# Kernel tuning notes

Measured on AMD Instinct MI355X. Metric: run time of the kernel, lower is better.

## Reference

```python
import jax, jax.numpy as jnp
import numpy as np

B, S, D, H, DH, R = 8, 2048, 1024, 16, 64, 32
ALPHA, BETA, GAMMA = 0.2, 0.1, 0.1


def setup_inputs() -> dict:
    key = jax.random.key(0)
    ks = jax.random.split(key, 5)
    x = jax.random.normal(ks[0], (B, S, D), jnp.float32)
    q = jax.random.normal(ks[1], (B, S, H, DH), jnp.float32)
    k = jax.random.normal(ks[2], (B, S, H, DH), jnp.float32)
    v_value = jax.random.normal(ks[3], (B, S, D), jnp.float32)
    # reentry_proj weight (orthogonal init approximated by scaled gaussian)
    W = jax.random.normal(ks[4], (D, D), jnp.float32) * np.float32(np.sqrt(0.5 / D))
    return {"x": x, "q": q, "k": k, "v_value": v_value, "W": W}


def _normalize(t):
    return t / (jnp.linalg.norm(t, axis=-1, keepdims=True) + 1e-6)


def reference(x, q, k, v_value, W):
    Bz, Sl, Dm = x.shape
    qf = q.reshape(Bz, Sl, Dm).transpose(1, 0, 2)        # (S, B, D)
    kf = k.reshape(Bz, Sl, Dm).transpose(1, 0, 2)        # (S, B, D)
    vf = v_value.transpose(1, 0, 2)                      # (S, B, D)
    U0 = jnp.zeros((Bz, R, Dm), x.dtype)
    V0 = jnp.zeros((Bz, R, Dm), x.dtype)

    def step(carry, inp):
        U, V = carry
        q_t, k_t, v_t = inp                              # each (B, D)
        U = (1.0 - ALPHA) * U + ALPHA * _normalize(q_t)[:, None, :]
        V = (1.0 - ALPHA) * V + ALPHA * _normalize(k_t)[:, None, :]
        # y_t = (U^T V) v_t, computed factorized: never materialize dim x dim
        s = jnp.einsum('brd,bd->br', V, v_t)             # (B, R)
        y = jnp.einsum('brd,br->bd', U, s)               # (B, D)
        n = jnp.maximum(jnp.linalg.norm(y, axis=-1, keepdims=True), 1e-6)
        y = y / (1.0 + BETA * (n - 1.0))                 # homeostasis
        fb = GAMMA * (y @ W.T)                           # reentry projection
        return (U, V), fb

    (_, _), fbs = jax.lax.scan(step, (U0, V0), (qf, kf, vf))
    return x + fbs.transpose(1, 0, 2)                    # (B, S, D)
```

## Files before the change

kernel.cpp:

```cpp
#include <hip/hip_runtime.h>
#include <hip/hip_bf16.h>
#include <cstdint>
#include <cstddef>

#define B_ 8
#define S_ 2048
#define D_ 1024
#define RFAC 32.0f
#define ALPHA 0.2f
#define BETA 0.1f
#define GAMMA 0.1f
#define KW 32
#define TB 64
#define PF_ 8

typedef float f32x4_t __attribute__((ext_vector_type(4)));
typedef short bf16x8_t __attribute__((ext_vector_type(8)));

__device__ __forceinline__ unsigned short f2bf(float f) {
    unsigned u = __float_as_uint(f);
    u = (u + 0x7fffu + ((u >> 16) & 1u)) >> 16;
    return (unsigned short)u;
}
__device__ __forceinline__ float bf2f(unsigned short h) {
    return __uint_as_float(((unsigned)h) << 16);
}

__global__ __launch_bounds__(256) void wconv_k(const float* __restrict__ W,
                                               unsigned short* __restrict__ Wb) {
    int i = blockIdx.x * 256 + threadIdx.x;
    float4 w = ((const float4*)W)[i];
    ushort4 o;
    o.x = f2bf(w.x); o.y = f2bf(w.y); o.z = f2bf(w.z); o.w = f2bf(w.w);
    ((ushort4*)Wb)[i] = o;
}

__global__ __launch_bounds__(256) void ema_fused_k(const float* __restrict__ q,
                                                   const float* __restrict__ kk,
                                                   const float* __restrict__ vv,
                                                   unsigned short* __restrict__ Ub,
                                                   float* __restrict__ coef) {
    __shared__ float smn[2][8];
    __shared__ float sm2[TB * 8];
    const int chunks = S_ / TB;
    int b  = blockIdx.x / chunks;
    int t0 = (blockIdx.x % chunks) * TB;
    int ts = t0 - KW; if (ts < 0) ts = 0;
    int tid = threadIdx.x;
    int lane = tid & 63, wave = tid >> 6;
    size_t bbase = (size_t)b * S_ * D_ + tid * 4;
    const float* qp = q + bbase;
    const float* kp = kk + bbase;
    const float* vp = vv + bbase;
    unsigned short* up = Ub + bbase;

    float4 pq[PF_], pk[PF_], pv[PF_];
#pragma unroll
    for (int j = 0; j < PF_; ++j) {
        size_t o = (size_t)(ts + j) * D_;
        pq[j] = *(const float4*)(qp + o);
        pk[j] = *(const float4*)(kp + o);
        if (ts + j >= t0) pv[j] = *(const float4*)(vp + o);
    }
    float u0 = 0.f, u1 = 0.f, u2 = 0.f, u3 = 0.f;
    float v0 = 0.f, v1 = 0.f, v2 = 0.f, v3 = 0.f;
    const float om = 1.f - ALPHA;
    const int NI = t0 + TB - ts;
    const int tend = t0 + TB;
    for (int g = 0; g < NI; g += PF_) {
#pragma unroll
        for (int j = 0; j < PF_; ++j) {
            int t = ts + g + j;
            int slot = t & 1;
            float sqq = pq[j].x * pq[j].x + pq[j].y * pq[j].y
                      + pq[j].z * pq[j].z + pq[j].w * pq[j].w;
            float sqk = pk[j].x * pk[j].x + pk[j].y * pk[j].y
                      + pk[j].z * pk[j].z + pk[j].w * pk[j].w;
#pragma unroll
            for (int off = 32; off > 0; off >>= 1) {
                sqq += __shfl_xor(sqq, off, 64);
                sqk += __shfl_xor(sqk, off, 64);
            }
            if (lane == 0) {
                smn[slot][wave * 2 + 0] = sqq;
                smn[slot][wave * 2 + 1] = sqk;
            }
            __syncthreads();
            float nq = smn[slot][0] + smn[slot][2] + smn[slot][4] + smn[slot][6];
            float nk = smn[slot][1] + smn[slot][3] + smn[slot][5] + smn[slot][7];
            float aq = ALPHA / (sqrtf(nq) + 1e-6f);
            float ak = ALPHA / (sqrtf(nk) + 1e-6f);
            u0 = om * u0 + aq * pq[j].x; u1 = om * u1 + aq * pq[j].y;
            u2 = om * u2 + aq * pq[j].z; u3 = om * u3 + aq * pq[j].w;
            v0 = om * v0 + ak * pk[j].x; v1 = om * v1 + ak * pk[j].y;
            v2 = om * v2 + ak * pk[j].z; v3 = om * v3 + ak * pk[j].w;
            if (t >= t0) {
                float uu = u0 * u0 + u1 * u1 + u2 * u2 + u3 * u3;
                float sd = v0 * pv[j].x + v1 * pv[j].y + v2 * pv[j].z + v3 * pv[j].w;
#pragma unroll
                for (int off = 32; off > 0; off >>= 1) {
                    uu += __shfl_xor(uu, off, 64);
                    sd += __shfl_xor(sd, off, 64);
                }
                if (lane == 0) {
                    sm2[(t - t0) * 8 + wave * 2 + 0] = uu;
                    sm2[(t - t0) * 8 + wave * 2 + 1] = sd;
                }
                ushort4 us;
                us.x = f2bf(u0); us.y = f2bf(u1); us.z = f2bf(u2); us.w = f2bf(u3);
                *(ushort4*)(up + (size_t)t * D_) = us;
            }
            int tf = t + PF_;
            int tc = tf < tend ? tf : tend - 1;
            size_t o2 = (size_t)tc * D_;
            pq[j] = *(const float4*)(qp + o2);
            pk[j] = *(const float4*)(kp + o2);
            if (tf >= t0) pv[j] = *(const float4*)(vp + o2);
        }
    }
    __syncthreads();
    if (tid < TB) {
        float uu = sm2[tid * 8 + 0] + sm2[tid * 8 + 2] + sm2[tid * 8 + 4] + sm2[tid * 8 + 6];
        float sd = sm2[tid * 8 + 1] + sm2[tid * 8 + 3] + sm2[tid * 8 + 5] + sm2[tid * 8 + 7];
        float nrm = RFAC * fabsf(sd) * sqrtf(uu);
        float n = fmaxf(nrm, 1e-6f);
        coef[b * S_ + t0 + tid] = GAMMA * RFAC * sd / (1.f + BETA * (n - 1.f));
    }
}

#define BM 128
#define BN 128
#define BK 64
#define NT (D_ / BK)

__global__ __launch_bounds__(256) void gemm_k(const unsigned short* __restrict__ A,
                                              const unsigned short* __restrict__ Bw,
                                              const float* __restrict__ coef,
                                              const float* __restrict__ x,
                                              float* __restrict__ out) {
    const int N = D_, K = D_;
    __shared__ unsigned short lds[2 * 2 * BM * BK];
    int bid = blockIdx.x;
    int swz = (bid & 7) * 128 + (bid >> 3);
    int tm = swz >> 3, tn = swz & 7;
    int m0 = tm * BM, n0 = tn * BN;
    int tid = threadIdx.x;
    int lane = tid & 63;
    int wid = tid >> 6;
    int wr = wid >> 1, wc = wid & 1;
    int lr = lane & 15, lg = lane >> 4;

    f32x4_t acc[4][4];
#pragma unroll
    for (int i = 0; i < 4; ++i)
#pragma unroll
        for (int j = 0; j < 4; ++j)
            acc[i][j] = (f32x4_t){0.f, 0.f, 0.f, 0.f};

#define STAGE_MAT(buf, kt, isB)                                                       \
    {                                                                                 \
        const unsigned short* Gp =                                                    \
            ((isB) ? Bw + (size_t)n0 * K : A + (size_t)m0 * K) + (size_t)(kt) * BK;   \
        char* Lp = (char*)lds + (buf) * 32768 + (isB) * 16384;                        \
        _Pragma("unroll")                                                             \
        for (int i = 0; i < 4; ++i) {                                                 \
            int c = i * 256 + tid;                                                    \
            int row = c >> 3, cl = c & 7;                                             \
            int gc = cl ^ (row & 7);                   \
            __builtin_amdgcn_global_load_lds(                                         \
                (const __attribute__((address_space(1))) void*)(Gp + (size_t)row * K + gc * 8), \
                (__attribute__((address_space(3))) void*)(Lp + c * 16), 16, 0, 0);    \
        }                                                                             \
    }
#define STAGE_TILE(buf, kt) STAGE_MAT(buf, kt, 0) STAGE_MAT(buf, kt, 1)

    STAGE_TILE(0, 0);
    STAGE_TILE(1, 1);

    for (int t = 0; t < NT; ++t) {
        if (t == NT - 1) asm volatile("s_waitcnt vmcnt(0)" ::: "memory");
        else             asm volatile("s_waitcnt vmcnt(8)" ::: "memory");
        __builtin_amdgcn_s_barrier();
        const unsigned short* La = lds + (t & 1) * 16384;
        const unsigned short* Lb = La + 8192;
        bf16x8_t af[4][2], bf[4][2];
#pragma unroll
        for (int kkk = 0; kkk < 2; ++kkk) {
#pragma unroll
            for (int mi = 0; mi < 4; ++mi) {
                int row = wr * 64 + mi * 16 + lr;
                int ch = (kkk * 4 + lg) ^ (row & 7);
                af[mi][kkk] = *(const bf16x8_t*)(La + (row * 8 + ch) * 8);
            }
#pragma unroll
            for (int ni = 0; ni < 4; ++ni) {
                int row = wc * 64 + ni * 16 + lr;
                int ch = (kkk * 4 + lg) ^ (row & 7);
                bf[ni][kkk] = *(const bf16x8_t*)(Lb + (row * 8 + ch) * 8);
            }
        }
        asm volatile("s_waitcnt lgkmcnt(0)" ::: "memory");
        __builtin_amdgcn_sched_barrier(0);
        __builtin_amdgcn_s_setprio(1);
#pragma unroll
        for (int kkk = 0; kkk < 2; ++kkk)
#pragma unroll
            for (int mi = 0; mi < 4; ++mi)
#pragma unroll
                for (int ni = 0; ni < 4; ++ni)
                    acc[mi][ni] = __builtin_amdgcn_mfma_f32_16x16x32_bf16(
                        af[mi][kkk], bf[ni][kkk], acc[mi][ni], 0, 0, 0);
        __builtin_amdgcn_s_setprio(0);
        __builtin_amdgcn_s_barrier();
        if (t + 2 < NT) { STAGE_TILE((t & 1), t + 2); }
    }
#undef STAGE_TILE
#undef STAGE_MAT

#pragma unroll
    for (int mi = 0; mi < 4; ++mi) {
#pragma unroll
        for (int i = 0; i < 4; ++i) {
            int m = m0 + wr * 64 + mi * 16 + lg * 4 + i;
            float cf = coef[m];
#pragma unroll
            for (int ni = 0; ni < 4; ++ni) {
                int n = n0 + wc * 64 + ni * 16 + lr;
                size_t idx = (size_t)m * N + n;
                out[idx] = x[idx] + cf * acc[mi][ni][i];
            }
        }
    }
}

extern "C" void kernel_launch(void* const* d_in, const int* in_sizes, int n_in,
                              void* d_out, int out_size, void* d_ws, size_t ws_size,
                              hipStream_t stream) {
    const float* x  = (const float*)d_in[0];
    const float* q  = (const float*)d_in[1];
    const float* k  = (const float*)d_in[2];
    const float* vv = (const float*)d_in[3];
    const float* W  = (const float*)d_in[4];
    float* out = (float*)d_out;

    const size_t M = (size_t)B_ * S_;
    char* ws = (char*)d_ws;
    unsigned short* Ub = (unsigned short*)ws;
    unsigned short* Wb = (unsigned short*)(ws + M * D_ * 2);
    float* coef = (float*)(ws + M * D_ * 2 + (size_t)D_ * D_ * 2);
    size_t needed = M * D_ * 2 + (size_t)D_ * D_ * 2 + M * 4;
    if (ws_size < needed) return;

    wconv_k<<<dim3((D_ * D_) / 1024), dim3(256), 0, stream>>>(W, Wb);
    ema_fused_k<<<dim3(B_ * (S_ / TB)), dim3(256), 0, stream>>>(q, k, vv, Ub, coef);
    gemm_k<<<dim3((M / BM) * (D_ / BN)), dim3(256), 0, stream>>>(Ub, Wb, coef, x, out);
}
```

Baseline: 139.8 us.

## Run EMA scan with one wavefront per chunk to remove block barriers

The EMA kernel now uses a single 64-lane wavefront per (batch, chunk), with each lane holding 16 elements. This replaces the per-timestep __syncthreads and LDS cross-wave reductions with pure shuffle reductions. The norm reductions for q and k are computed two steps ahead to hide shuffle latency, coef is written directly by lane 0, and bf16 packing uses v_cvt_pk_bf16_f32. The cost is only 256 single-wave blocks, so memory-level parallelism per CU drops and register pressure rises.

After: 173.0 us. 1.24x slower.

```diff
diff --git a/kernel.cpp b/kernel.cpp
--- a/kernel.cpp
+++ b/kernel.cpp
@@ -12,7 +12,6 @@
 #define GAMMA 0.1f
 #define KW 32
 #define TB 64
-#define PF_ 8
 
 typedef float f32x4_t __attribute__((ext_vector_type(4)));
 typedef short bf16x8_t __attribute__((ext_vector_type(8)));
@@ -22,8 +21,10 @@
     u = (u + 0x7fffu + ((u >> 16) & 1u)) >> 16;
     return (unsigned short)u;
 }
-__device__ __forceinline__ float bf2f(unsigned short h) {
-    return __uint_as_float(((unsigned)h) << 16);
+__device__ __forceinline__ unsigned cvtpk(float lo, float hi) {
+    unsigned r;
+    asm("v_cvt_pk_bf16_f32 %0, %1, %2" : "=v"(r) : "v"(lo), "v"(hi));
+    return r;
 }
 
 __global__ __launch_bounds__(256) void wconv_k(const float* __restrict__ W,
@@ -35,96 +36,122 @@
     ((ushort4*)Wb)[i] = o;
 }
 
-__global__ __launch_bounds__(256) void ema_fused_k(const float* __restrict__ q,
-                                                   const float* __restrict__ kk,
-                                                   const float* __restrict__ vv,
-                                                   unsigned short* __restrict__ Ub,
-                                                   float* __restrict__ coef) {
-    __shared__ float smn[2][8];
-    __shared__ float sm2[TB * 8];
-    const int chunks = S_ / TB;
-    int b  = blockIdx.x / chunks;
-    int t0 = (blockIdx.x % chunks) * TB;
+__global__ __launch_bounds__(64, 1) void ema_fused_k(const float* __restrict__ q,
+                                                     const float* __restrict__ kk,
+                                                     const float* __restrict__ vv,
+                                                     unsigned short* __restrict__ Ub,
+                                                     float* __restrict__ coef) {
+    int lane = threadIdx.x;
+    int b = blockIdx.x >> 5;
+    int chunk = blockIdx.x & 31;
+    int t0 = chunk * TB;
     int ts = t0 - KW; if (ts < 0) ts = 0;
-    int tid = threadIdx.x;
-    int lane = tid & 63, wave = tid >> 6;
-    size_t bbase = (size_t)b * S_ * D_ + tid * 4;
-    const float* qp = q + bbase;
-    const float* kp = kk + bbase;
-    const float* vp = vv + bbase;
-    unsigned short* up = Ub + bbase;
-
-    float4 pq[PF_], pk[PF_], pv[PF_];
-#pragma unroll
-    for (int j = 0; j < PF_; ++j) {
-        size_t o = (size_t)(ts + j) * D_;
-        pq[j] = *(const float4*)(qp + o);
-        pk[j] = *(const float4*)(kp + o);
-        if (ts + j >= t0) pv[j] = *(const float4*)(vp + o);
-    }
-    float u0 = 0.f, u1 = 0.f, u2 = 0.f, u3 = 0.f;
-    float v0 = 0.f, v1 = 0.f, v2 = 0.f, v3 = 0.f;
+    const int tend = t0 + TB;
+    const float4* qb = (const float4*)(q  + (size_t)b * S_ * D_) + lane;
+    const float4* kb = (const float4*)(kk + (size_t)b * S_ * D_) + lane;
+    const float4* vb = (const float4*)(vv + (size_t)b * S_ * D_) + lane;
+
+    float4 rq[4][4], rk[4][4], rv[4][4];
+    float nqs[4], nks[4];
+
+#pragma unroll
+    for (int j = 0; j < 4; ++j) {
+        size_t o = (size_t)(ts + j) * 256;
+#pragma unroll
+        for (int i = 0; i < 4; ++i) { rq[j][i] = qb[o + i * 64]; rk[j][i] = kb[o + i * 64]; }
+        if (ts + j >= t0) {
+#pragma unroll
+            for (int i = 0; i < 4; ++i) rv[j][i] = vb[o + i * 64];
+        }
+    }
+#pragma unroll
+    for (int m = 0; m < 2; ++m) {
+        float sq = 0.f, sk = 0.f;
+#pragma unroll
+        for (int i = 0; i < 4; ++i) {
+            sq += rq[m][i].x*rq[m][i].x + rq[m][i].y*rq[m][i].y + rq[m][i].z*rq[m][i].z + rq[m][i].w*rq[m][i].w;
+            sk += rk[m][i].x*rk[m][i].x + rk[m][i].y*rk[m][i].y + rk[m][i].z*rk[m][i].z + rk[m][i].w*rk[m][i].w;
+        }
+#pragma unroll
+        for (int off = 32; off > 0; off >>= 1) {
+            sq += __shfl_xor(sq, off, 64);
+            sk += __shfl_xor(sk, off, 64);
+        }
+        nqs[m] = sq; nks[m] = sk;
+    }
+
+    float4 u4[4], v4[4];
+#pragma unroll
+    for (int i = 0; i < 4; ++i) {
+        u4[i] = (float4){0.f,0.f,0.f,0.f};
+        v4[i] = (float4){0.f,0.f,0.f,0.f};
+    }
     const float om = 1.f - ALPHA;
-    const int NI = t0 + TB - ts;
-    const int tend = t0 + TB;
-    for (int g = 0; g < NI; g += PF_) {
-#pragma unroll
-        for (int j = 0; j < PF_; ++j) {
+    const int NI = tend - ts;
+    for (int g = 0; g < NI; g += 4) {
+#pragma unroll
+        for (int j = 0; j < 4; ++j) {
             int t = ts + g + j;
-            int slot = t & 1;
-            float sqq = pq[j].x * pq[j].x + pq[j].y * pq[j].y
-                      + pq[j].z * pq[j].z + pq[j].w * pq[j].w;
-            float sqk = pk[j].x * pk[j].x + pk[j].y * pk[j].y
-                      + pk[j].z * pk[j].z + pk[j].w * pk[j].w;
-#pragma unroll
-            for (int off = 32; off > 0; off >>= 1) {
-                sqq += __shfl_xor(sqq, off, 64);
-                sqk += __shfl_xor(sqk, off, 64);
-            }
-            if (lane == 0) {
-                smn[slot][wave * 2 + 0] = sqq;
-                smn[slot][wave * 2 + 1] = sqk;
-            }
-            __syncthreads();
-            float nq = smn[slot][0] + smn[slot][2] + smn[slot][4] + smn[slot][6];
-            float nk = smn[slot][1] + smn[slot][3] + smn[slot][5] + smn[slot][7];
-            float aq = ALPHA / (sqrtf(nq) + 1e-6f);
-            float ak = ALPHA / (sqrtf(nk) + 1e-6f);
-            u0 = om * u0 + aq * pq[j].x; u1 = om * u1 + aq * pq[j].y;
-            u2 = om * u2 + aq * pq[j].z; u3 = om * u3 + aq * pq[j].w;
-            v0 = om * v0 + ak * pk[j].x; v1 = om * v1 + ak * pk[j].y;
-            v2 = om * v2 + ak * pk[j].z; v3 = om * v3 + ak * pk[j].w;
+            if (t + 2 < tend) {
+                const int s = (j + 2) & 3;
+                float sq = 0.f, sk = 0.f;
+#pragma unroll
+                for (int i = 0; i < 4; ++i) {
+                    sq += rq[s][i].x*rq[s][i].x + rq[s][i].y*rq[s][i].y + rq[s][i].z*rq[s][i].z + rq[s][i].w*rq[s][i].w;
+                    sk += rk[s][i].x*rk[s][i].x + rk[s][i].y*rk[s][i].y + rk[s][i].z*rk[s][i].z + rk[s][i].w*rk[s][i].w;
+                }
+#pragma unroll
+                for (int off = 32; off > 0; off >>= 1) {
+                    sq += __shfl_xor(sq, off, 64);
+                    sk += __shfl_xor(sk, off, 64);
+                }
+                nqs[s] = sq; nks[s] = sk;
+            }
+            float aq = ALPHA / (sqrtf(nqs[j]) + 1e-6f);
+            float ak = ALPHA / (sqrtf(nks[j]) + 1e-6f);
+#pragma unroll
+            for (int i = 0; i < 4; ++i) {
+                u4[i].x = om*u4[i].x + aq*rq[j][i].x; u4[i].y = om*u4[i].y + aq*rq[j][i].y;
+                u4[i].z = om*u4[i].z + aq*rq[j][i].z; u4[i].w = om*u4[i].w + aq*rq[j][i].w;
+                v4[i].x = om*v4[i].x + ak*rk[j][i].x; v4[i].y = om*v4[i].y + ak*rk[j][i].y;
+                v4[i].z = om*v4[i].z + ak*rk[j][i].z; v4[i].w = om*v4[i].w + ak*rk[j][i].w;
+            }
             if (t >= t0) {
-                float uu = u0 * u0 + u1 * u1 + u2 * u2 + u3 * u3;
-                float sd = v0 * pv[j].x + v1 * pv[j].y + v2 * pv[j].z + v3 * pv[j].w;
+                float uu = 0.f, sd = 0.f;
+#pragma unroll
+                for (int i = 0; i < 4; ++i) {
+                    uu += u4[i].x*u4[i].x + u4[i].y*u4[i].y + u4[i].z*u4[i].z + u4[i].w*u4[i].w;
+                    sd += v4[i].x*rv[j][i].x + v4[i].y*rv[j][i].y + v4[i].z*rv[j][i].z + v4[i].w*rv[j][i].w;
+                }
 #pragma unroll
                 for (int off = 32; off > 0; off >>= 1) {
                     uu += __shfl_xor(uu, off, 64);
                     sd += __shfl_xor(sd, off, 64);
                 }
                 if (lane == 0) {
-                    sm2[(t - t0) * 8 + wave * 2 + 0] = uu;
-                    sm2[(t - t0) * 8 + wave * 2 + 1] = sd;
-                }
-                ushort4 us;
-                us.x = f2bf(u0); us.y = f2bf(u1); us.z = f2bf(u2); us.w = f2bf(u3);
-                *(ushort4*)(up + (size_t)t * D_) = us;
-            }
-            int tf = t + PF_;
+                    float nrm = RFAC * fabsf(sd) * sqrtf(uu);
+                    float n = fmaxf(nrm, 1e-6f);
+                    coef[b * S_ + t] = GAMMA * RFAC * sd / (1.f + BETA * (n - 1.f));
+                }
+                unsigned short* ur = Ub + (size_t)(b * S_ + t) * D_ + lane * 4;
+#pragma unroll
+                for (int i = 0; i < 4; ++i) {
+                    uint2 rr;
+                    rr.x = cvtpk(u4[i].x, u4[i].y);
+                    rr.y = cvtpk(u4[i].z, u4[i].w);
+                    *(uint2*)(ur + i * 256) = rr;
+                }
+            }
+            int tf = t + 4;
             int tc = tf < tend ? tf : tend - 1;
-            size_t o2 = (size_t)tc * D_;
-            pq[j] = *(const float4*)(qp + o2);
-            pk[j] = *(const float4*)(kp + o2);
-            if (tf >= t0) pv[j] = *(const float4*)(vp + o2);
-        }
-    }
-    __syncthreads();
-    if (tid < TB) {
-        float uu = sm2[tid * 8 + 0] + sm2[tid * 8 + 2] + sm2[tid * 8 + 4] + sm2[tid * 8 + 6];
-        float sd = sm2[tid * 8 + 1] + sm2[tid * 8 + 3] + sm2[tid * 8 + 5] + sm2[tid * 8 + 7];
-        float nrm = RFAC * fabsf(sd) * sqrtf(uu);
-        float n = fmaxf(nrm, 1e-6f);
-        coef[b * S_ + t0 + tid] = GAMMA * RFAC * sd / (1.f + BETA * (n - 1.f));
+            size_t o = (size_t)tc * 256;
+#pragma unroll
+            for (int i = 0; i < 4; ++i) { rq[j][i] = qb[o + i * 64]; rk[j][i] = kb[o + i * 64]; }
+            if (tf >= t0 && tf < tend) {
+#pragma unroll
+                for (int i = 0; i < 4; ++i) rv[j][i] = vb[o + i * 64];
+            }
+        }
     }
 }
 
@@ -252,6 +279,6 @@
     if (ws_size < needed) return;
 
     wconv_k<<<dim3((D_ * D_) / 1024), dim3(256), 0, stream>>>(W, Wb);
-    ema_fused_k<<<dim3(B_ * (S_ / TB)), dim3(256), 0, stream>>>(q, k, vv, Ub, coef);
+    ema_fused_k<<<dim3(B_ * (S_ / TB)), dim3(64), 0, stream>>>(q, k, vv, Ub, coef);
     gemm_k<<<dim3((M / BM) * (D_ / BN)), dim3(256), 0, stream>>>(Ub, Wb, coef, x, out);
 }
```
